# Performance work log

Hardware: AMD Instinct MI355X
Metric: run time of the kernel (lower is better)

## Reference

```python
import jax, jax.numpy as jnp
import numpy as np

N_NODES, N_EDGES = 50000, 800000
D_NODE, D_EDGE, N_CLASSES, N_HEADS = 64, 64, 40, 4


def setup_inputs() -> dict:
    key = jax.random.key(0)
    ks = jax.random.split(key, 20)
    g = lambda k, shp: (jax.random.normal(k, shp, jnp.float32) * (1.0 / np.sqrt(shp[0])))
    inp = {
        "nodes": jax.random.normal(ks[0], (N_NODES, D_NODE), jnp.float32),
        "edges": jax.random.normal(ks[1], (N_EDGES, D_EDGE), jnp.float32),
        "edge_index": jax.random.randint(ks[2], (2, N_EDGES), 0, N_NODES, jnp.int32),
        # NodeAttention params
        "Wq_n": g(ks[3], (D_NODE, D_NODE)),
        "Wk_n": g(ks[4], (D_NODE, D_NODE)),
        "We_n": g(ks[5], (D_EDGE, D_NODE)),
        "Wv_n": g(ks[6], (D_NODE, D_NODE)),
        "Wo_n": g(ks[7], (D_NODE, D_NODE)),
        # EdgeAttention params
        "Wq_e": g(ks[8], (D_EDGE, D_EDGE)),
        "Wk_e": g(ks[9], (D_EDGE, D_EDGE)),
        "Wn_e": g(ks[10], (D_NODE, D_EDGE)),
        "Wv_e": g(ks[11], (D_EDGE, D_EDGE)),
        "Wo_e": g(ks[12], (D_EDGE, D_EDGE)),
        # classifier: Linear(2*d_node+d_edge -> d_edge), GELU, Linear(d_edge -> num_classes)
        "W1": g(ks[13], (2 * D_NODE + D_EDGE, D_EDGE)),
        "b1": jnp.zeros((D_EDGE,), jnp.float32),
        "W2": g(ks[14], (D_EDGE, N_CLASSES)),
        "b2": jnp.zeros((N_CLASSES,), jnp.float32),
    }
    return inp


def _segment_softmax(scores, seg, num_segments):
    # scores: [E, H], seg: [E] -> softmax over edges within each segment
    m = jax.ops.segment_max(scores, seg, num_segments)
    ex = jnp.exp(scores - m[seg])
    den = jax.ops.segment_sum(ex, seg, num_segments)
    return ex / (den[seg] + 1e-9)


def _forward(nodes, edges, edge_index, Wq_n, Wk_n, We_n, Wv_n, Wo_n,
             Wq_e, Wk_e, Wn_e, Wv_e, Wo_e, W1, b1, W2, b2):
    src, tgt = edge_index[0], edge_index[1]
    E = edges.shape[0]
    N = nodes.shape[0]
    Dh_n = D_NODE // N_HEADS
    Dh_e = D_EDGE // N_HEADS

    # ---- NodeAttention: nodes attend over incoming edges ----
    q = (nodes @ Wq_n).reshape(N, N_HEADS, Dh_n)
    k = ((nodes @ Wk_n)[src] + edges @ We_n).reshape(E, N_HEADS, Dh_n)
    v = (nodes @ Wv_n)[src].reshape(E, N_HEADS, Dh_n)
    s_n = (q[tgt] * k).sum(-1) / jnp.sqrt(jnp.float32(Dh_n))  # [E, H]
    a_n = _segment_softmax(s_n, tgt, N)
    msg = jax.ops.segment_sum(a_n[..., None] * v, tgt, N).reshape(N, D_NODE)
    new_nodes = nodes + msg @ Wo_n

    # ---- EdgeAttention: edges attend among edges sharing a source node ----
    qe = (edges @ Wq_e).reshape(E, N_HEADS, Dh_e)
    ke = (edges @ Wk_e + nodes[src] @ Wn_e).reshape(E, N_HEADS, Dh_e)
    ve = (edges @ Wv_e).reshape(E, N_HEADS, Dh_e)
    s_e = (qe * ke).sum(-1) / jnp.sqrt(jnp.float32(Dh_e))  # [E, H]
    a_e = _segment_softmax(s_e, src, N)
    pooled = jax.ops.segment_sum(a_e[..., None] * ve, src, N).reshape(N, D_EDGE)
    new_edges = edges + pooled[src] @ Wo_e

    # ---- edge-indexed gather + concat + 2-layer GELU MLP classifier ----
    combined = jnp.concatenate([new_nodes[src], new_nodes[tgt], new_edges], axis=-1)
    h = jax.nn.gelu(combined @ W1 + b1)
    return h @ W2 + b2  # [E, num_classes]


def reference(nodes, edges, edge_index, Wq_n, Wk_n, We_n, Wv_n, Wo_n,
              Wq_e, Wk_e, Wn_e, Wv_e, Wo_e, W1, b1, W2, b2):
    return _forward(nodes, edges, edge_index, Wq_n, Wk_n, We_n, Wv_n, Wo_n,
                    Wq_e, Wk_e, Wn_e, Wv_e, Wo_e, W1, b1, W2, b2)
```

## Files before the change

### kernel.cpp

```cpp
#include <hip/hip_runtime.h>
#include <cstdint>
#include <cstddef>

typedef unsigned short u16t;
typedef __attribute__((ext_vector_type(8))) short bf16x8;
typedef __attribute__((ext_vector_type(4))) float f32x4;

#define NNODES 50000
#define NEDGES 800000
#define NP 50176

#define MFMA(a, b, c) __builtin_amdgcn_mfma_f32_16x16x32_bf16((a), (b), (c), 0, 0, 0)

__device__ inline float b2f(short s) {
    union { float f; unsigned int u; } c;
    c.u = ((unsigned int)(unsigned short)s) << 16;
    return c.f;
}
__device__ inline short f2b(float f) {
    union { float f; unsigned int u; } c; c.f = f;
    unsigned int u = c.u;
    unsigned int r = (u + 0x7FFFu + ((u >> 16) & 1u)) >> 16;
    return (short)(unsigned short)r;
}
__device__ inline f32x4 zero4() { f32x4 z = {0.f, 0.f, 0.f, 0.f}; return z; }

__device__ inline bf16x8 ld8f(const float* p) {
    float4 a = *(const float4*)p;
    float4 b = *(const float4*)(p + 4);
    bf16x8 r;
    r[0] = f2b(a.x); r[1] = f2b(a.y); r[2] = f2b(a.z); r[3] = f2b(a.w);
    r[4] = f2b(b.x); r[5] = f2b(b.y); r[6] = f2b(b.z); r[7] = f2b(b.w);
    return r;
}
__device__ inline bf16x8 ld8fs(const float* p, float s) {
    float4 a = *(const float4*)p;
    float4 b = *(const float4*)(p + 4);
    bf16x8 r;
    r[0] = f2b(a.x * s); r[1] = f2b(a.y * s); r[2] = f2b(a.z * s); r[3] = f2b(a.w * s);
    r[4] = f2b(b.x * s); r[5] = f2b(b.y * s); r[6] = f2b(b.z * s); r[7] = f2b(b.w * s);
    return r;
}

__device__ inline float gelu_f(float x) {
    float u = 0.7978845608028654f * (x + 0.044715f * x * x * x);
    float e = __expf(2.f * u);
    return 0.5f * x * (2.f - 2.f / (e + 1.f));
}

__device__ inline float tree16(float* a, int l) {
#pragma unroll
    for (int b = 0; b < 4; ++b) {
        const int m = 1 << b;
        const bool up = (l & m) != 0;
#pragma unroll
        for (int j = 0; j < (8 >> b); ++j) {
            float keep = up ? a[2 * j + 1] : a[2 * j];
            float send = up ? a[2 * j] : a[2 * j + 1];
            a[j] = keep + __shfl_xor(send, m);
        }
    }
    return a[0];
}

__global__ void k_init(float* __restrict__ msg, float* __restrict__ pooled,
                       float* __restrict__ d_n, float* __restrict__ d_e) {
    int i = blockIdx.x * 256 + threadIdx.x;
    if (i < NP * 64) { msg[i] = 0.f; pooled[i] = 0.f; }
    if (i < NP * 4)  { d_n[i] = 0.f; d_e[i] = 0.f; }
}

__global__ __launch_bounds__(256) void k_node_proj(
        const float* __restrict__ nodes,
        const float* __restrict__ Wq, const float* __restrict__ Wk,
        const float* __restrict__ Wv, const float* __restrict__ Wn,
        u16t* __restrict__ qn, u16t* __restrict__ kn,
        u16t* __restrict__ vn, u16t* __restrict__ nWn) {
    __shared__ __align__(16) u16t wt[256 * 72];
    {
        const float* Ws[4] = {Wq, Wk, Wv, Wn};
        for (int g = 0; g < 4; ++g) {
            const float* W = Ws[g];
            u16t* dst = wt + g * 64 * 72;
            for (int idx = threadIdx.x; idx < 4096; idx += 256) {
                int n = idx & 63, k = idx >> 6;
                dst[n * 72 + k] = (u16t)f2b(W[idx]);
            }
        }
    }
    __syncthreads();
    int l = threadIdx.x & 63, w = threadIdx.x >> 6;
    int q = l >> 4, c = l & 15;
    int r0 = blockIdx.x * 256 + w * 64;

    bf16x8 A[4][2];
#pragma unroll
    for (int st = 0; st < 4; ++st) {
        int row = r0 + st * 16 + c;
        if (row >= NNODES) row = NNODES - 1;
#pragma unroll
        for (int ks = 0; ks < 2; ++ks)
            A[st][ks] = ld8f(nodes + (size_t)row * 64 + ks * 32 + q * 8);
    }
    u16t* outs[4] = {qn, kn, vn, nWn};
    for (int cg = 0; cg < 4; ++cg) {
        bf16x8 B[2][4];
#pragma unroll
        for (int ks = 0; ks < 2; ++ks)
#pragma unroll
            for (int t = 0; t < 4; ++t)
                B[ks][t] = *(const bf16x8*)(wt + (cg * 64 + t * 16 + c) * 72 + ks * 32 + q * 8);
        float scale = (cg == 0) ? 0.25f : 1.0f;
        u16t* out = outs[cg];
#pragma unroll
        for (int st = 0; st < 4; ++st) {
            f32x4 acc[4];
#pragma unroll
            for (int t = 0; t < 4; ++t) acc[t] = zero4();
#pragma unroll
            for (int ks = 0; ks < 2; ++ks)
#pragma unroll
                for (int t = 0; t < 4; ++t)
                    acc[t] = MFMA(A[st][ks], B[ks][t], acc[t]);
#pragma unroll
            for (int r = 0; r < 4; ++r) {
                int row = r0 + st * 16 + q * 4 + r;
                if (row < NNODES) {
#pragma unroll
                    for (int t = 0; t < 4; ++t)
                        out[(size_t)row * 64 + t * 16 + c] = (u16t)f2b(acc[t][r] * scale);
                }
            }
        }
    }
}

__global__ __launch_bounds__(256) void k_edge_fused(
        const float* __restrict__ edges, const int* __restrict__ eidx,
        const float* __restrict__ WeN, const float* __restrict__ WqE,
        const float* __restrict__ WkE, const float* __restrict__ WvE,
        const u16t* __restrict__ qn, const u16t* __restrict__ kn,
        const u16t* __restrict__ nWn, const u16t* __restrict__ vn,
        float* __restrict__ d_n, float* __restrict__ d_e,
        float* __restrict__ msg, float* __restrict__ pooled) {
    __shared__ __align__(16) u16t wt[256 * 72];
    for (int idx = threadIdx.x; idx < 4096; idx += 256) {
        int n = idx & 63, k = idx >> 6;
        wt[n * 72 + k]         = (u16t)f2b(WeN[idx]);
        wt[(64 + n) * 72 + k]  = (u16t)f2b(0.25f * WqE[idx]);
        wt[(128 + n) * 72 + k] = (u16t)f2b(WkE[idx]);
        wt[(192 + n) * 72 + k] = (u16t)f2b(WvE[idx]);
    }
    __syncthreads();
    int l = threadIdx.x & 63, w = threadIdx.x >> 6;
    int q = l >> 4, c = l & 15;
    int e0 = blockIdx.x * 256 + w * 64;

    for (int st = 0; st < 4; ++st) {
        int ebase = e0 + st * 16;
        int eA = ebase + c;
        bf16x8 A0 = ld8f(edges + (size_t)eA * 64 + q * 8);
        bf16x8 A1 = ld8f(edges + (size_t)eA * 64 + 32 + q * 8);

        int sr_[4], tg_[4];
#pragma unroll
        for (int r = 0; r < 4; ++r) {
            int e = ebase + q * 4 + r;
            sr_[r] = eidx[e];
            tg_[r] = eidx[NEDGES + e];
        }
        int eL = ebase + (l >> 2), hL = l & 3;
        int srL = eidx[eL], tgL = eidx[NEDGES + eL];

        f32x4 aQe[4], aKe[4];
#pragma unroll
        for (int t = 0; t < 4; ++t) { aQe[t] = zero4(); aKe[t] = zero4(); }
#pragma unroll
        for (int t = 0; t < 4; ++t) {
            const u16t* b1 = wt + (64 + t * 16 + c) * 72;
            const u16t* b2 = wt + (128 + t * 16 + c) * 72;
            aQe[t] = MFMA(A0, *(const bf16x8*)(b1 + q * 8), aQe[t]);
            aQe[t] = MFMA(A1, *(const bf16x8*)(b1 + 32 + q * 8), aQe[t]);
            aKe[t] = MFMA(A0, *(const bf16x8*)(b2 + q * 8), aKe[t]);
            aKe[t] = MFMA(A1, *(const bf16x8*)(b2 + 32 + q * 8), aKe[t]);
        }
        float pe[16];
#pragma unroll
        for (int r = 0; r < 4; ++r)
#pragma unroll
            for (int t = 0; t < 4; ++t) {
                int col = t * 16 + c;
                float ng = b2f((short)nWn[(size_t)sr_[r] * 64 + col]);
                pe[r * 4 + t] = aQe[t][r] * (aKe[t][r] + ng);
            }
        float exe = __expf(tree16(pe, l));
        unsafeAtomicAdd(&d_e[srL * 4 + hL], exe);

        f32x4 aVe[4];
#pragma unroll
        for (int t = 0; t < 4; ++t) aVe[t] = zero4();
#pragma unroll
        for (int t = 0; t < 4; ++t) {
            const u16t* b3 = wt + (192 + t * 16 + c) * 72;
            aVe[t] = MFMA(A0, *(const bf16x8*)(b3 + q * 8), aVe[t]);
            aVe[t] = MFMA(A1, *(const bf16x8*)(b3 + 32 + q * 8), aVe[t]);
        }
#pragma unroll
        for (int r = 0; r < 4; ++r)
#pragma unroll
            for (int t = 0; t < 4; ++t) {
                float a = __shfl(exe, (l & 48) + r * 4 + t);
                unsafeAtomicAdd(&pooled[(size_t)sr_[r] * 64 + t * 16 + c], a * aVe[t][r]);
            }

        f32x4 aWe[4];
#pragma unroll
        for (int t = 0; t < 4; ++t) aWe[t] = zero4();
#pragma unroll
        for (int t = 0; t < 4; ++t) {
            const u16t* b0 = wt + (t * 16 + c) * 72;
            aWe[t] = MFMA(A0, *(const bf16x8*)(b0 + q * 8), aWe[t]);
            aWe[t] = MFMA(A1, *(const bf16x8*)(b0 + 32 + q * 8), aWe[t]);
        }
        float pn[16];
#pragma unroll
        for (int r = 0; r < 4; ++r)
#pragma unroll
            for (int t = 0; t < 4; ++t) {
                int col = t * 16 + c;
                float qg = b2f((short)qn[(size_t)tg_[r] * 64 + col]);
                float kg = b2f((short)kn[(size_t)sr_[r] * 64 + col]);
                pn[r * 4 + t] = qg * (kg + aWe[t][r]);
            }
        float exn = __expf(tree16(pn, l));
        unsafeAtomicAdd(&d_n[tgL * 4 + hL], exn);

#pragma unroll
        for (int el = 0; el < 16; ++el) {
            int sE = __shfl(srL, el << 2);
            int tE = __shfl(tgL, el << 2);
            float a = __shfl(exn, (el << 2) + (l >> 4));
            float vv = b2f((short)vn[(size_t)sE * 64 + l]);
            unsafeAtomicAdd(&msg[(size_t)tE * 64 + l], a * vv);
        }
    }
}

__global__ __launch_bounds__(256) void k_node_update(
        const float* __restrict__ Ain, const float* __restrict__ den,
        const float* __restrict__ W, const float* __restrict__ base,
        u16t* __restrict__ out) {
    __shared__ __align__(16) u16t wt[64 * 72];
    for (int idx = threadIdx.x; idx < 4096; idx += 256) {
        int n = idx & 63, k = idx >> 6;
        wt[n * 72 + k] = (u16t)f2b(W[idx]);
    }
    __syncthreads();
    int l = threadIdx.x & 63, w = threadIdx.x >> 6;
    int q = l >> 4, c = l & 15;
    int r0 = blockIdx.x * 256 + w * 64;
    bf16x8 B[2][4];
#pragma unroll
    for (int ks = 0; ks < 2; ++ks)
#pragma unroll
        for (int t = 0; t < 4; ++t)
            B[ks][t] = *(const bf16x8*)(wt + (t * 16 + c) * 72 + ks * 32 + q * 8);
    for (int st = 0; st < 4; ++st) {
        int row = r0 + st * 16 + c;
        if (row >= NNODES) row = NNODES - 1;
        bf16x8 A[2];
#pragma unroll
        for (int ks = 0; ks < 2; ++ks) {
            float iv = 1.f / (den[row * 4 + ks * 2 + (q >> 1)] + 1e-9f);
            A[ks] = ld8fs(Ain + (size_t)row * 64 + ks * 32 + q * 8, iv);
        }
        f32x4 acc[4];
#pragma unroll
        for (int t = 0; t < 4; ++t) acc[t] = zero4();
#pragma unroll
        for (int t = 0; t < 4; ++t) {
            acc[t] = MFMA(A[0], B[0][t], acc[t]);
            acc[t] = MFMA(A[1], B[1][t], acc[t]);
        }
#pragma unroll
        for (int r = 0; r < 4; ++r) {
            int rw = r0 + st * 16 + q * 4 + r;
            if (rw < NNODES) {
#pragma unroll
                for (int t = 0; t < 4; ++t) {
                    int col = t * 16 + c;
                    float v = acc[t][r];
                    if (base) v += base[(size_t)rw * 64 + col];
                    out[(size_t)rw * 64 + col] = (u16t)f2b(v);
                }
            }
        }
    }
}

__global__ __launch_bounds__(256) void k_classifier(
        const float* __restrict__ edges, const int* __restrict__ eidx,
        const u16t* __restrict__ newN, const u16t* __restrict__ pWo,
        const float* __restrict__ W1, const float* __restrict__ b1,
        const float* __restrict__ W2, const float* __restrict__ b2,
        float* __restrict__ out) {
    __shared__ __align__(16) u16t wt1[64 * 200];
    __shared__ __align__(16) u16t wt2[48 * 72];
    __shared__ __align__(16) u16t hbuf[4][16 * 72];
    for (int idx = threadIdx.x; idx < 192 * 64; idx += 256) {
        int n = idx & 63, k = idx >> 6;
        wt1[n * 200 + k] = (u16t)f2b(W1[idx]);
    }
    for (int idx = threadIdx.x; idx < 48 * 64; idx += 256) {
        int n = idx % 48, k = idx / 48;
        wt2[n * 72 + k] = (n < 40) ? (u16t)f2b(W2[k * 40 + n]) : (u16t)0;
    }
    __syncthreads();
    int l = threadIdx.x & 63, w = threadIdx.x >> 6;
    int q = l >> 4, c = l & 15;
    int e0 = blockIdx.x * 256 + w * 64;

    bf16x8 B1[6][4];
#pragma unroll
    for (int ks = 0; ks < 6; ++ks)
#pragma unroll
        for (int t = 0; t < 4; ++t)
            B1[ks][t] = *(const bf16x8*)(wt1 + (t * 16 + c) * 200 + ks * 32 + q * 8);
    bf16x8 B2[2][3];
#pragma unroll
    for (int ks = 0; ks < 2; ++ks)
#pragma unroll
        for (int t = 0; t < 3; ++t)
            B2[ks][t] = *(const bf16x8*)(wt2 + (t * 16 + c) * 72 + ks * 32 + q * 8);

    for (int st = 0; st < 4; ++st) {
        int em = e0 + st * 16 + c;
        int srm = eidx[em], tgm = eidx[NEDGES + em];
        bf16x8 A[6];
#pragma unroll
        for (int ks = 0; ks < 2; ++ks) {
            A[ks]     = *(const bf16x8*)(newN + (size_t)srm * 64 + ks * 32 + q * 8);
            A[2 + ks] = *(const bf16x8*)(newN + (size_t)tgm * 64 + ks * 32 + q * 8);
            const float* ep = edges + (size_t)em * 64 + ks * 32 + q * 8;
            float4 x0 = *(const float4*)ep;
            float4 x1 = *(const float4*)(ep + 4);
            bf16x8 y = *(const bf16x8*)(pWo + (size_t)srm * 64 + ks * 32 + q * 8);
            bf16x8 z;
            z[0] = f2b(x0.x + b2f(y[0])); z[1] = f2b(x0.y + b2f(y[1]));
            z[2] = f2b(x0.z + b2f(y[2])); z[3] = f2b(x0.w + b2f(y[3]));
            z[4] = f2b(x1.x + b2f(y[4])); z[5] = f2b(x1.y + b2f(y[5]));
            z[6] = f2b(x1.z + b2f(y[6])); z[7] = f2b(x1.w + b2f(y[7]));
            A[4 + ks] = z;
        }
        f32x4 acc1[4];
#pragma unroll
        for (int t = 0; t < 4; ++t) acc1[t] = zero4();
#pragma unroll
        for (int ks = 0; ks < 6; ++ks)
#pragma unroll
            for (int t = 0; t < 4; ++t)
                acc1[t] = MFMA(A[ks], B1[ks][t], acc1[t]);
#pragma unroll
        for (int t = 0; t < 4; ++t) {
            float bb = b1[t * 16 + c];
#pragma unroll
            for (int r = 0; r < 4; ++r) {
                float x = acc1[t][r] + bb;
                hbuf[w][(q * 4 + r) * 72 + t * 16 + c] = (u16t)f2b(gelu_f(x));
            }
        }
        bf16x8 A2[2];
#pragma unroll
        for (int ks = 0; ks < 2; ++ks)
            A2[ks] = *(const bf16x8*)(&hbuf[w][c * 72 + ks * 32 + q * 8]);
        f32x4 acc2[3];
#pragma unroll
        for (int t = 0; t < 3; ++t) acc2[t] = zero4();
#pragma unroll
        for (int ks = 0; ks < 2; ++ks)
#pragma unroll
            for (int t = 0; t < 3; ++t)
                acc2[t] = MFMA(A2[ks], B2[ks][t], acc2[t]);
#pragma unroll
        for (int r = 0; r < 4; ++r) {
            int e = e0 + st * 16 + q * 4 + r;
#pragma unroll
            for (int t = 0; t < 3; ++t) {
                int col = t * 16 + c;
                if (col < 40)
                    out[(size_t)e * 40 + col] = acc2[t][r] + b2[col];
            }
        }
    }
}

extern "C" void kernel_launch(void* const* d_in, const int* in_sizes, int n_in,
                              void* d_out, int out_size, void* d_ws, size_t ws_size,
                              hipStream_t stream) {
    if (n_in < 17) return;
    const float* nodes = (const float*)d_in[0];
    const float* edges = (const float*)d_in[1];
    const int*   eidx  = (const int*)d_in[2];
    const float* Wq_n = (const float*)d_in[3];
    const float* Wk_n = (const float*)d_in[4];
    const float* We_n = (const float*)d_in[5];
    const float* Wv_n = (const float*)d_in[6];
    const float* Wo_n = (const float*)d_in[7];
    const float* Wq_e = (const float*)d_in[8];
    const float* Wk_e = (const float*)d_in[9];
    const float* Wn_e = (const float*)d_in[10];
    const float* Wv_e = (const float*)d_in[11];
    const float* Wo_e = (const float*)d_in[12];
    const float* W1   = (const float*)d_in[13];
    const float* b1   = (const float*)d_in[14];
    const float* W2   = (const float*)d_in[15];
    const float* b2   = (const float*)d_in[16];
    float* out = (float*)d_out;

    float* ws = (float*)d_ws;
    size_t o = 0;
    u16t* qn  = (u16t*)(ws + o); o += (size_t)NP * 32;
    u16t* kn  = (u16t*)(ws + o); o += (size_t)NP * 32;
    u16t* vn  = (u16t*)(ws + o); o += (size_t)NP * 32;
    u16t* nWn = (u16t*)(ws + o); o += (size_t)NP * 32;
    float* d_n = ws + o; o += (size_t)NP * 4;
    float* d_e = ws + o; o += (size_t)NP * 4;
    float* msg    = ws + o; o += (size_t)NP * 64;
    float* pooled = ws + o; o += (size_t)NP * 64;
    u16t* newN = (u16t*)(ws + o); o += (size_t)NP * 32;
    u16t* pWo  = (u16t*)(ws + o); o += (size_t)NP * 32;
    if (ws_size < o * sizeof(float)) return;

    k_init<<<12544, 256, 0, stream>>>(msg, pooled, d_n, d_e);
    k_node_proj<<<196, 256, 0, stream>>>(nodes, Wq_n, Wk_n, Wv_n, Wn_e, qn, kn, vn, nWn);
    k_edge_fused<<<3125, 256, 0, stream>>>(edges, eidx, We_n, Wq_e, Wk_e, Wv_e,
                                           qn, kn, nWn, vn, d_n, d_e, msg, pooled);
    k_node_update<<<196, 256, 0, stream>>>(msg, d_n, Wo_n, nodes, newN);
    k_node_update<<<196, 256, 0, stream>>>(pooled, d_e, Wo_e, nullptr, pWo);
    k_classifier<<<3125, 256, 0, stream>>>(edges, eidx, newN, pWo, W1, b1, W2, b2, out);
}
```

Measured before the change: 1.085 ms.

## Replace atomic scatter aggregation with CSR-sorted per-node gather

Builds CSR offsets for targets and sources each call (histogram, scan, fill) and splits the fused edge kernel into a score kernel that writes exp-scores per edge and a gather kernel where one wavefront per node reduces its incoming and outgoing edges. This removes the heavy float atomics into msg, pooled and the denominators, and folds the softmax normalisation into the gather. In exchange it adds six small preprocessing kernels with integer atomics, extra score buffers, and recomputes the V projection for source-grouped edges via random edge-row gathers.

```diff
diff --git a/kernel.cpp b/kernel.cpp
--- a/kernel.cpp
+++ b/kernel.cpp
@@ -33,14 +33,6 @@
     r[4] = f2b(b.x); r[5] = f2b(b.y); r[6] = f2b(b.z); r[7] = f2b(b.w);
     return r;
 }
-__device__ inline bf16x8 ld8fs(const float* p, float s) {
-    float4 a = *(const float4*)p;
-    float4 b = *(const float4*)(p + 4);
-    bf16x8 r;
-    r[0] = f2b(a.x * s); r[1] = f2b(a.y * s); r[2] = f2b(a.z * s); r[3] = f2b(a.w * s);
-    r[4] = f2b(b.x * s); r[5] = f2b(b.y * s); r[6] = f2b(b.z * s); r[7] = f2b(b.w * s);
-    return r;
-}
 
 __device__ inline float gelu_f(float x) {
     float u = 0.7978845608028654f * (x + 0.044715f * x * x * x);
@@ -63,11 +55,70 @@
     return a[0];
 }
 
-__global__ void k_init(float* __restrict__ msg, float* __restrict__ pooled,
-                       float* __restrict__ d_n, float* __restrict__ d_e) {
+__device__ inline int wscan_incl(int v) {
+    int l = threadIdx.x & 63;
+#pragma unroll
+    for (int d = 1; d < 64; d <<= 1) {
+        int t = __shfl_up(v, d);
+        if (l >= d) v += t;
+    }
+    return v;
+}
+
+__global__ void k_zero(int* __restrict__ cnt) {
     int i = blockIdx.x * 256 + threadIdx.x;
-    if (i < NP * 64) { msg[i] = 0.f; pooled[i] = 0.f; }
-    if (i < NP * 4)  { d_n[i] = 0.f; d_e[i] = 0.f; }
+    cnt[i] = 0;
+}
+
+__global__ void k_hist(const int* __restrict__ eidx, int* __restrict__ cnt) {
+    int e = blockIdx.x * 256 + threadIdx.x;
+    int sr = eidx[e], tg = eidx[NEDGES + e];
+    atomicAdd(&cnt[tg], 1);
+    atomicAdd(&cnt[NP + sr], 1);
+}
+
+__global__ void k_scan_blk(const int* __restrict__ cnt, int* __restrict__ incl,
+                           int* __restrict__ tot) {
+    __shared__ int wsum[4];
+    int i = blockIdx.x * 256 + threadIdx.x;
+    int v = cnt[i];
+    int sc = wscan_incl(v);
+    int w = threadIdx.x >> 6;
+    if ((threadIdx.x & 63) == 63) wsum[w] = sc;
+    __syncthreads();
+    int off = 0;
+    for (int k = 0; k < w; ++k) off += wsum[k];
+    incl[i] = sc + off;
+    if (threadIdx.x == 255) tot[blockIdx.x] = sc + off;
+}
+
+__global__ void k_scan_top(const int* __restrict__ tot, int* __restrict__ ttop) {
+    __shared__ int wsum[8];
+    int i = threadIdx.x;
+    int v = (i < 392) ? tot[i] : 0;
+    int sc = wscan_incl(v);
+    int w = threadIdx.x >> 6;
+    if ((threadIdx.x & 63) == 63) wsum[w] = sc;
+    __syncthreads();
+    int off = 0;
+    for (int k = 0; k < w; ++k) off += wsum[k];
+    if (i < 392) ttop[i] = sc + off - v;
+}
+
+__global__ void k_scan_add(const int* __restrict__ cnt, const int* __restrict__ incl,
+                           const int* __restrict__ ttop, int* __restrict__ ofs,
+                           int* __restrict__ cur) {
+    int i = blockIdx.x * 256 + threadIdx.x;
+    int v = incl[i] - cnt[i] + ttop[blockIdx.x];
+    ofs[i] = v; cur[i] = v;
+}
+
+__global__ void k_fill(const int* __restrict__ eidx, int* __restrict__ cur,
+                       int* __restrict__ perm) {
+    int e = blockIdx.x * 256 + threadIdx.x;
+    int sr = eidx[e], tg = eidx[NEDGES + e];
+    perm[atomicAdd(&cur[tg], 1)] = e;
+    perm[atomicAdd(&cur[NP + sr], 1)] = e;
 }
 
 __global__ __launch_bounds__(256) void k_node_proj(
@@ -135,21 +186,17 @@
     }
 }
 
-__global__ __launch_bounds__(256) void k_edge_fused(
+__global__ __launch_bounds__(256) void k_edge_scores(
         const float* __restrict__ edges, const int* __restrict__ eidx,
-        const float* __restrict__ WeN, const float* __restrict__ WqE,
-        const float* __restrict__ WkE, const float* __restrict__ WvE,
-        const u16t* __restrict__ qn, const u16t* __restrict__ kn,
-        const u16t* __restrict__ nWn, const u16t* __restrict__ vn,
-        float* __restrict__ d_n, float* __restrict__ d_e,
-        float* __restrict__ msg, float* __restrict__ pooled) {
-    __shared__ __align__(16) u16t wt[256 * 72];
+        const float* __restrict__ WeN, const float* __restrict__ WqE, const float* __restrict__ WkE,
+        const u16t* __restrict__ qn, const u16t* __restrict__ kn, const u16t* __restrict__ nWn,
+        float* __restrict__ s_n, float* __restrict__ s_e) {
+    __shared__ __align__(16) u16t wt[192 * 72];
     for (int idx = threadIdx.x; idx < 4096; idx += 256) {
         int n = idx & 63, k = idx >> 6;
         wt[n * 72 + k]         = (u16t)f2b(WeN[idx]);
         wt[(64 + n) * 72 + k]  = (u16t)f2b(0.25f * WqE[idx]);
         wt[(128 + n) * 72 + k] = (u16t)f2b(WkE[idx]);
-        wt[(192 + n) * 72 + k] = (u16t)f2b(WvE[idx]);
     }
     __syncthreads();
     int l = threadIdx.x & 63, w = threadIdx.x >> 6;
@@ -169,8 +216,6 @@
             sr_[r] = eidx[e];
             tg_[r] = eidx[NEDGES + e];
         }
-        int eL = ebase + (l >> 2), hL = l & 3;
-        int srL = eidx[eL], tgL = eidx[NEDGES + eL];
 
         f32x4 aQe[4], aKe[4];
 #pragma unroll
@@ -193,25 +238,7 @@
                 float ng = b2f((short)nWn[(size_t)sr_[r] * 64 + col]);
                 pe[r * 4 + t] = aQe[t][r] * (aKe[t][r] + ng);
             }
-        float exe = __expf(tree16(pe, l));
-        unsafeAtomicAdd(&d_e[srL * 4 + hL], exe);
-
-        f32x4 aVe[4];
-#pragma unroll
-        for (int t = 0; t < 4; ++t) aVe[t] = zero4();
-#pragma unroll
-        for (int t = 0; t < 4; ++t) {
-            const u16t* b3 = wt + (192 + t * 16 + c) * 72;
-            aVe[t] = MFMA(A0, *(const bf16x8*)(b3 + q * 8), aVe[t]);
-            aVe[t] = MFMA(A1, *(const bf16x8*)(b3 + 32 + q * 8), aVe[t]);
-        }
-#pragma unroll
-        for (int r = 0; r < 4; ++r)
-#pragma unroll
-            for (int t = 0; t < 4; ++t) {
-                float a = __shfl(exe, (l & 48) + r * 4 + t);
-                unsafeAtomicAdd(&pooled[(size_t)sr_[r] * 64 + t * 16 + c], a * aVe[t][r]);
-            }
+        s_e[(size_t)ebase * 4 + l] = __expf(tree16(pe, l));
 
         f32x4 aWe[4];
 #pragma unroll
@@ -232,24 +259,94 @@
                 float kg = b2f((short)kn[(size_t)sr_[r] * 64 + col]);
                 pn[r * 4 + t] = qg * (kg + aWe[t][r]);
             }
-        float exn = __expf(tree16(pn, l));
-        unsafeAtomicAdd(&d_n[tgL * 4 + hL], exn);
-
-#pragma unroll
-        for (int el = 0; el < 16; ++el) {
-            int sE = __shfl(srL, el << 2);
-            int tE = __shfl(tgL, el << 2);
-            float a = __shfl(exn, (el << 2) + (l >> 4));
-            float vv = b2f((short)vn[(size_t)sE * 64 + l]);
-            unsafeAtomicAdd(&msg[(size_t)tE * 64 + l], a * vv);
-        }
+        s_n[(size_t)ebase * 4 + l] = __expf(tree16(pn, l));
+    }
+}
+
+__global__ __launch_bounds__(256) void k_gather(
+        const float* __restrict__ edges, const int* __restrict__ eidx,
+        const float* __restrict__ WvE,
+        const int* __restrict__ ofs, const int* __restrict__ cnt,
+        const int* __restrict__ perm,
+        const float* __restrict__ s_n, const float* __restrict__ s_e,
+        const u16t* __restrict__ vn,
+        float* __restrict__ msg, float* __restrict__ pooled) {
+    __shared__ __align__(16) u16t wt[64 * 72];
+    for (int idx = threadIdx.x; idx < 4096; idx += 256) {
+        int n = idx & 63, k = idx >> 6;
+        wt[n * 72 + k] = (u16t)f2b(WvE[idx]);
+    }
+    __syncthreads();
+    int l = threadIdx.x & 63;
+    int q = l >> 4, c = l & 15;
+    int gw = (blockIdx.x * 256 + (int)threadIdx.x) >> 6;
+    if (gw >= NNODES) return;
+
+    {
+        int o0 = ofs[gw], n0 = cnt[gw];
+        float acc = 0.f, den = 0.f;
+        int e = (n0 > 0) ? perm[o0] : 0;
+        for (int j = 0; j < n0; ++j) {
+            int sr = eidx[e];
+            int en = (j + 1 < n0) ? perm[o0 + j + 1] : 0;
+            float a = s_n[(size_t)e * 4 + q];
+            den += a;
+            acc += a * b2f((short)vn[(size_t)sr * 64 + l]);
+            e = en;
+        }
+        msg[(size_t)gw * 64 + l] = acc / (den + 1e-9f);
+    }
+
+    {
+        int o1 = ofs[NP + gw], n1 = cnt[NP + gw];
+        float part[4] = {0.f, 0.f, 0.f, 0.f};
+        float dpart[4] = {0.f, 0.f, 0.f, 0.f};
+        for (int j0 = 0; j0 < n1; j0 += 16) {
+            int rem = n1 - j0;
+            int cc = (c < rem) ? c : (rem - 1);
+            int eC = perm[o1 + j0 + cc];
+            bf16x8 A0 = ld8f(edges + (size_t)eC * 64 + q * 8);
+            bf16x8 A1 = ld8f(edges + (size_t)eC * 64 + 32 + q * 8);
+            f32x4 acc4[4];
+#pragma unroll
+            for (int t = 0; t < 4; ++t) acc4[t] = zero4();
+#pragma unroll
+            for (int t = 0; t < 4; ++t) {
+                const u16t* bp = wt + (t * 16 + c) * 72;
+                acc4[t] = MFMA(A0, *(const bf16x8*)(bp + q * 8), acc4[t]);
+                acc4[t] = MFMA(A1, *(const bf16x8*)(bp + 32 + q * 8), acc4[t]);
+            }
+#pragma unroll
+            for (int r = 0; r < 4; ++r) {
+                int row = q * 4 + r;
+                int eR = __shfl(eC, row);
+                float4 a4;
+                if (row < rem) a4 = *(const float4*)(s_e + (size_t)eR * 4);
+                else           { a4.x = 0.f; a4.y = 0.f; a4.z = 0.f; a4.w = 0.f; }
+                float ar[4] = {a4.x, a4.y, a4.z, a4.w};
+#pragma unroll
+                for (int t = 0; t < 4; ++t) {
+                    part[t] += ar[t] * acc4[t][r];
+                    dpart[t] += ar[t];
+                }
+            }
+        }
+#pragma unroll
+        for (int t = 0; t < 4; ++t) {
+            part[t] += __shfl_xor(part[t], 16);
+            part[t] += __shfl_xor(part[t], 32);
+            dpart[t] += __shfl_xor(dpart[t], 16);
+            dpart[t] += __shfl_xor(dpart[t], 32);
+        }
+        float pv = (q == 0) ? part[0] : (q == 1) ? part[1] : (q == 2) ? part[2] : part[3];
+        float dv = (q == 0) ? dpart[0] : (q == 1) ? dpart[1] : (q == 2) ? dpart[2] : dpart[3];
+        pooled[(size_t)gw * 64 + l] = pv / (dv + 1e-9f);
     }
 }
 
 __global__ __launch_bounds__(256) void k_node_update(
-        const float* __restrict__ Ain, const float* __restrict__ den,
-        const float* __restrict__ W, const float* __restrict__ base,
-        u16t* __restrict__ out) {
+        const float* __restrict__ Ain, const float* __restrict__ W,
+        const float* __restrict__ base, u16t* __restrict__ out) {
     __shared__ __align__(16) u16t wt[64 * 72];
     for (int idx = threadIdx.x; idx < 4096; idx += 256) {
         int n = idx & 63, k = idx >> 6;
@@ -270,10 +367,8 @@
         if (row >= NNODES) row = NNODES - 1;
         bf16x8 A[2];
 #pragma unroll
-        for (int ks = 0; ks < 2; ++ks) {
-            float iv = 1.f / (den[row * 4 + ks * 2 + (q >> 1)] + 1e-9f);
-            A[ks] = ld8fs(Ain + (size_t)row * 64 + ks * 32 + q * 8, iv);
-        }
+        for (int ks = 0; ks < 2; ++ks)
+            A[ks] = ld8f(Ain + (size_t)row * 64 + ks * 32 + q * 8);
         f32x4 acc[4];
 #pragma unroll
         for (int t = 0; t < 4; ++t) acc[t] = zero4();
@@ -423,19 +518,33 @@
     u16t* kn  = (u16t*)(ws + o); o += (size_t)NP * 32;
     u16t* vn  = (u16t*)(ws + o); o += (size_t)NP * 32;
     u16t* nWn = (u16t*)(ws + o); o += (size_t)NP * 32;
-    float* d_n = ws + o; o += (size_t)NP * 4;
-    float* d_e = ws + o; o += (size_t)NP * 4;
+    float* s_n = ws + o; o += (size_t)NEDGES * 4;
+    float* s_e = ws + o; o += (size_t)NEDGES * 4;
     float* msg    = ws + o; o += (size_t)NP * 64;
     float* pooled = ws + o; o += (size_t)NP * 64;
     u16t* newN = (u16t*)(ws + o); o += (size_t)NP * 32;
     u16t* pWo  = (u16t*)(ws + o); o += (size_t)NP * 32;
+    int* cnt  = (int*)(ws + o); o += (size_t)2 * NP;
+    int* incl = (int*)(ws + o); o += (size_t)2 * NP;
+    int* ofs  = (int*)(ws + o); o += (size_t)2 * NP;
+    int* cur  = (int*)(ws + o); o += (size_t)2 * NP;
+    int* tot  = (int*)(ws + o); o += 512;
+    int* ttop = (int*)(ws + o); o += 512;
+    int* perm = (int*)(ws + o); o += (size_t)2 * NEDGES;
     if (ws_size < o * sizeof(float)) return;
 
-    k_init<<<12544, 256, 0, stream>>>(msg, pooled, d_n, d_e);
+    k_zero<<<392, 256, 0, stream>>>(cnt);
+    k_hist<<<3125, 256, 0, stream>>>(eidx, cnt);
+    k_scan_blk<<<392, 256, 0, stream>>>(cnt, incl, tot);
+    k_scan_top<<<1, 512, 0, stream>>>(tot, ttop);
+    k_scan_add<<<392, 256, 0, stream>>>(cnt, incl, ttop, ofs, cur);
+    k_fill<<<3125, 256, 0, stream>>>(eidx, cur, perm);
     k_node_proj<<<196, 256, 0, stream>>>(nodes, Wq_n, Wk_n, Wv_n, Wn_e, qn, kn, vn, nWn);
-    k_edge_fused<<<3125, 256, 0, stream>>>(edges, eidx, We_n, Wq_e, Wk_e, Wv_e,
-                                           qn, kn, nWn, vn, d_n, d_e, msg, pooled);
-    k_node_update<<<196, 256, 0, stream>>>(msg, d_n, Wo_n, nodes, newN);
-    k_node_update<<<196, 256, 0, stream>>>(pooled, d_e, Wo_e, nullptr, pWo);
+    k_edge_scores<<<3125, 256, 0, stream>>>(edges, eidx, We_n, Wq_e, Wk_e,
+                                            qn, kn, nWn, s_n, s_e);
+    k_gather<<<12500, 256, 0, stream>>>(edges, eidx, Wv_e, ofs, cnt, perm,
+                                        s_n, s_e, vn, msg, pooled);
+    k_node_update<<<196, 256, 0, stream>>>(msg, Wo_n, nodes, newN);
+    k_node_update<<<196, 256, 0, stream>>>(pooled, Wo_e, nullptr, pWo);
     k_classifier<<<3125, 256, 0, stream>>>(edges, eidx, newN, pWo, W1, b1, W2, b2, out);
 }
```

Result: faster. 1.055 ms (-2.7%).
